# Kernel tuning notes

Hardware: AMD Instinct MI355X
Metric: run time of the kernel (lower is better)

The kernel has to match this reference:

```python
import jax, jax.numpy as jnp
import numpy as np

B, S, H, P = 8, 2048, 512, 16
K = H // 2

def setup_inputs() -> dict:
    key = jax.random.key(0)
    ks = jax.random.split(key, 6)
    sc_h = 1.0 / np.sqrt(H)
    sc_k = 1.0 / np.sqrt(K)
    return {
        "hidden_state": jax.random.normal(ks[0], (B, S, H), dtype=jnp.float32),
        "head_w": jax.random.normal(ks[1], (P, H), dtype=jnp.float32) * sc_h,
        "head_b": jnp.zeros((P,), dtype=jnp.float32),
        "embeds": jax.random.normal(ks[2], (P, H), dtype=jnp.float32),
        "w1": jax.random.normal(ks[3], (P, H, K), dtype=jnp.float32) * sc_h,
        "b1": jnp.zeros((P, K), dtype=jnp.float32),
        "w2": jax.random.normal(ks[4], (P, K, H), dtype=jnp.float32) * sc_k,
        "b2": jnp.zeros((P, H), dtype=jnp.float32),
    }

def reference(hidden_state, head_w, head_b, embeds, w1, b1, w2, b2):
    # Routing: pool over seq, linear head, softmax over programs -> (B, P)
    pooled = hidden_state.mean(axis=1)                      # (B, H)
    logits = jnp.einsum("bh,ph->bp", pooled, head_w) + head_b
    probs = jax.nn.softmax(logits, axis=-1)                  # (B, P)

    # Add program embedding per expert: (P, B, S, H)
    x = hidden_state[None, :, :, :] + embeds[:, None, None, :]
    # Expert MLP: Linear(H->K), exact GELU, Linear(K->H)
    mid = jax.nn.gelu(
        jnp.einsum("pbsh,phk->pbsk", x, w1) + b1[:, None, None, :],
        approximate=False,
    )
    adapted = jnp.einsum("pbsk,pkh->pbsh", mid, w2) + b2[:, None, None, :]
    # Weighted sum over programs with per-batch probs
    out = jnp.einsum("pbsh,bp->bsh", adapted, probs)         # (B, S, H)
    return out
```

## Files before the change

### kernel.cpp

```cpp
#include <hip/hip_runtime.h>
#include <hip/hip_bf16.h>
#include <stdint.h>

#define B_ 8
#define S_ 2048
#define H_ 512
#define P_ 16
#define K_ 256
#define M_TOT (B_*S_)
#define KCAT (P_*K_)

typedef short bf8v __attribute__((ext_vector_type(8)));
typedef float f4v  __attribute__((ext_vector_type(4)));

__device__ __align__(16) unsigned short g_hidden[M_TOT*H_];
__device__ __align__(16) unsigned short g_w1t[P_*K_*H_];
__device__ __align__(16) unsigned short g_w2cat[H_*KCAT];
__device__ __align__(16) unsigned short g_mid[(size_t)M_TOT*KCAT];
__device__ float g_bias1[P_*K_];
__device__ float g_probs[B_*P_];
__device__ float g_bias2w[B_*H_];

__device__ __forceinline__ unsigned short f2bf(float x){
  unsigned int u = __builtin_bit_cast(unsigned int, x);
  u += 0x7fffu + ((u >> 16) & 1u);
  return (unsigned short)(u >> 16);
}

__device__ __forceinline__ float gelu_prob(float x, float prob){
  float x2 = x*x;
  float t1 = 0.044715f*x;
  float u2 = fmaf(t1, x2, x);
  float e  = __expf(1.5957691216f*u2);
  float r  = __builtin_amdgcn_rcpf(e + 1.0f);
  float px = prob*x;
  return fmaf(-px, r, px);
}

__device__ __forceinline__ void gll16(const unsigned short* src, unsigned short* lds){
  __builtin_amdgcn_global_load_lds(
      (const __attribute__((address_space(1))) unsigned int*)src,
      (__attribute__((address_space(3))) unsigned int*)lds,
      16, 0, 0);
}

__global__ void cvt_pool(const float* __restrict__ hs, float* __restrict__ pooled){
  const int row0 = blockIdx.x * 64;
  const int b = row0 >> 11;
  const int tx = threadIdx.x & 127, ty = threadIdx.x >> 7;
  const float4* src = (const float4*)(hs + (size_t)row0*H_) + tx;
  ushort4* dst = (ushort4*)g_hidden + (size_t)row0*(H_/4) + tx;
  float4 s = {0.f,0.f,0.f,0.f};
  for (int r = ty; r < 64; r += 2){
    float4 v = src[(size_t)r*128];
    s.x += v.x; s.y += v.y; s.z += v.z; s.w += v.w;
    ushort4 o = {f2bf(v.x), f2bf(v.y), f2bf(v.z), f2bf(v.w)};
    dst[(size_t)r*128] = o;
  }
  __shared__ float4 red[256];
  red[threadIdx.x] = s;
  __syncthreads();
  if (ty == 0){
    float4 a = red[threadIdx.x], c = red[threadIdx.x + 128];
    atomicAdd(&pooled[b*H_ + tx*4 + 0], a.x + c.x);
    atomicAdd(&pooled[b*H_ + tx*4 + 1], a.y + c.y);
    atomicAdd(&pooled[b*H_ + tx*4 + 2], a.z + c.z);
    atomicAdd(&pooled[b*H_ + tx*4 + 3], a.w + c.w);
  }
}

__global__ void routing_kernel(const float* __restrict__ pooled,
                               const float* __restrict__ head_w,
                               const float* __restrict__ head_b,
                               const float* __restrict__ b2,
                               const float* __restrict__ b1){
  __shared__ float logits[B_][P_];
  __shared__ float sprob[B_][P_];
  int w = threadIdx.x >> 6, lane = threadIdx.x & 63;
  for (int idx = threadIdx.x; idx < P_*K_; idx += blockDim.x)
    g_bias1[idx] = b1[idx];
  for (int i = 0; i < 16; ++i){
    int pair = w*16 + i; int b = pair >> 4; int p = pair & 15;
    float acc = 0.0f;
    for (int h = lane; h < H_; h += 64) acc += pooled[b*H_+h]*head_w[p*H_+h];
    for (int off=32; off; off>>=1) acc += __shfl_down(acc, off);
    if (lane==0) logits[b][p] = acc * (1.0f/S_) + head_b[p];
  }
  __syncthreads();
  if (threadIdx.x < B_){
    int b = threadIdx.x;
    float mx = -1e30f;
    #pragma unroll
    for (int p=0;p<P_;++p) mx = fmaxf(mx, logits[b][p]);
    float e[P_]; float s = 0.0f;
    #pragma unroll
    for (int p=0;p<P_;++p){ e[p] = __expf(logits[b][p]-mx); s += e[p]; }
    float inv = 1.0f/s;
    #pragma unroll
    for (int p=0;p<P_;++p){ float pr = e[p]*inv; g_probs[b*P_+p] = pr; sprob[b][p] = pr; }
  }
  __syncthreads();
  for (int idx = threadIdx.x; idx < B_*H_; idx += blockDim.x){
    int b = idx >> 9, h = idx & (H_-1);
    float a = 0.0f;
    #pragma unroll
    for (int p=0;p<P_;++p) a += sprob[b][p]*b2[p*H_+h];
    g_bias2w[idx] = a;
  }
}

__global__ void transpose_cvt(const float* __restrict__ in, int R, int C, int which,
                              const float* __restrict__ embeds){
  int nrt = R >> 5, nct = C >> 5;
  int p   = blockIdx.x / (nrt*nct);
  int rem = blockIdx.x % (nrt*nct);
  int rt = rem / nct, ct = rem % nct;
  int tx = threadIdx.x & 31, ty = threadIdx.x >> 5;
  __shared__ float t[32][33];
  const float* ip = in + (size_t)p*R*C + (size_t)(rt*32 + ty)*C + ct*32 + tx;
  #pragma unroll
  for (int k=0;k<4;++k) t[ty + 8*k][tx] = ip[(size_t)8*k*C];
  __syncthreads();
  if (which == 0){
    unsigned short* op = g_w1t + (size_t)p*R*C + (size_t)(ct*32 + ty)*R + rt*32 + tx;
    #pragma unroll
    for (int k=0;k<4;++k) op[(size_t)8*k*R] = f2bf(t[tx][ty + 8*k]);
    if (ty == 0){
      float s = 0.0f;
      const float* ep = embeds + p*H_ + rt*32;
      #pragma unroll 8
      for (int hh=0; hh<32; ++hh) s = fmaf(ep[hh], t[hh][tx], s);
      atomicAdd(&g_bias1[p*K_ + ct*32 + tx], s);
    }
  } else {
    unsigned short* op = g_w2cat + (size_t)(ct*32 + ty)*KCAT + p*K_ + rt*32 + tx;
    #pragma unroll
    for (int k=0;k<4;++k) op[(size_t)8*k*KCAT] = f2bf(t[tx][ty + 8*k]);
  }
}


__device__ __forceinline__ void stage128(unsigned short* dst, const unsigned short* gsrc,
                                         int strideShorts, int koff, int tid){
  #pragma unroll
  for (int s = 0; s < 4; ++s){
    const int o   = (s*256 + tid)*8;
    const int row = o >> 6;
    const int ku  = (o & 63) >> 3;
    const int sku = ku ^ (row & 7);
    gll16(gsrc + (size_t)row*strideShorts + koff + sku*8, dst + o);
  }
}

__device__ __forceinline__ void kcompute(const unsigned short* Ab, const unsigned short* Bb,
    int rowA0, int rowB0, int l15, int lhi, f4v acc[4][4]){
  #pragma unroll
  for (int ksub=0; ksub<2; ++ksub){
    const int kb = ksub*64 + lhi*16;
    bf8v aF[4], bF[4];
    #pragma unroll
    for (int t=0; t<4; ++t){
      const int ra = rowA0 + t*16 + l15;
      aF[t] = *(const bf8v*)((const char*)Ab + ra*128 + (kb ^ ((ra&7)<<4)));
      const int rb = rowB0 + t*16 + l15;
      bF[t] = *(const bf8v*)((const char*)Bb + rb*128 + (kb ^ ((rb&7)<<4)));
    }
    __builtin_amdgcn_s_setprio(1);
    #pragma unroll
    for (int mt=0; mt<4; ++mt)
      #pragma unroll
      for (int nt=0; nt<4; ++nt)
        acc[mt][nt] = __builtin_amdgcn_mfma_f32_16x16x32_bf16(aF[mt], bF[nt], acc[mt][nt], 0,0,0);
    __builtin_amdgcn_s_setprio(0);
  }
}

__global__ __launch_bounds__(256, 2) void l1_kernel(){
  __shared__ __align__(16) unsigned short lds[4*128*64];
  const int bid = blockIdx.x;
  const int xcd = bid & 7, i = bid >> 3;
  const int n0 = (xcd*4 + (i&3)) * 128;
  const int m0 = (i >> 2) * 128;
  const int p = n0 >> 8;
  const int b = m0 >> 11;
  const int tid = threadIdx.x, w = tid >> 6, lane = tid & 63;
  const int wm = w >> 1, wn = w & 1, l15 = lane & 15, lhi = lane >> 4;
  const unsigned short* gA = g_hidden + (size_t)m0 * H_;
  const unsigned short* gB = g_w1t + (size_t)n0 * H_;

  f4v acc[4][4];
  #pragma unroll
  for (int a=0;a<4;++a)
    #pragma unroll
    for (int c=0;c<4;++c) acc[a][c] = {0.f,0.f,0.f,0.f};

  stage128(lds, gA, H_, 0, tid);
  stage128(lds + 16384, gB, H_, 0, tid);
  __syncthreads();
  for (int kt = 0; kt < 8; ++kt){
    const int cur = kt & 1;
    unsigned short* An = lds + (cur ? 0 : 8192);
    unsigned short* Bn = lds + 16384 + (cur ? 0 : 8192);
    const unsigned short* Ac = lds + (cur ? 8192 : 0);
    const unsigned short* Bc = lds + 16384 + (cur ? 8192 : 0);
    if (kt < 7){
      stage128(An, gA, H_, (kt+1)*64, tid);
      stage128(Bn, gB, H_, (kt+1)*64, tid);
    }
    kcompute(Ac, Bc, wm*64, wn*64, l15, lhi, acc);
    __syncthreads();
  }

  const float prob = g_probs[b*P_ + p];
  #pragma unroll
  for (int nt=0; nt<4; ++nt){
    const int col = wn*64 + nt*16 + l15;
    const float bias = g_bias1[n0 + col];
    #pragma unroll
    for (int mt=0; mt<4; ++mt){
      #pragma unroll
      for (int j=0;j<4;++j){
        const int row = wm*64 + mt*16 + lhi*4 + j;
        float v = acc[mt][nt][j] + bias;
        lds[row*136 + col] = f2bf(gelu_prob(v, prob));
      }
    }
  }
  __syncthreads();
  const int cc = tid & 15, rr = tid >> 4;
  #pragma unroll
  for (int pass=0; pass<8; ++pass){
    const int row = pass*16 + rr;
    bf8v vv = *(const bf8v*)&lds[row*136 + cc*8];
    *(bf8v*)&g_mid[(size_t)(m0+row)*KCAT + n0 + cc*8] = vv;
  }
}

__global__ __launch_bounds__(256, 2) void l2_kernel(float* __restrict__ out){
  __shared__ __align__(16) unsigned short lds[4*128*64];
  const int bid = blockIdx.x;
  const int xcd = bid & 7, i = bid >> 3;
  const int n0 = (i & 3) * 128;
  const int m0 = (xcd*16 + (i >> 2)) * 128;
  const int b = m0 >> 11;
  const int tid = threadIdx.x, w = tid >> 6, lane = tid & 63;
  const int wm = w >> 1, wn = w & 1, l15 = lane & 15, lhi = lane >> 4;
  const unsigned short* gA = g_mid + (size_t)m0 * KCAT;
  const unsigned short* gB = g_w2cat + (size_t)n0 * KCAT;

  f4v acc[4][4];
  #pragma unroll
  for (int a=0;a<4;++a)
    #pragma unroll
    for (int c=0;c<4;++c) acc[a][c] = {0.f,0.f,0.f,0.f};

  stage128(lds, gA, KCAT, 0, tid);
  stage128(lds + 16384, gB, KCAT, 0, tid);
  __syncthreads();
  for (int kt = 0; kt < 64; ++kt){
    const int cur = kt & 1;
    unsigned short* An = lds + (cur ? 0 : 8192);
    unsigned short* Bn = lds + 16384 + (cur ? 0 : 8192);
    const unsigned short* Ac = lds + (cur ? 8192 : 0);
    const unsigned short* Bc = lds + 16384 + (cur ? 8192 : 0);
    if (kt < 63){
      stage128(An, gA, KCAT, (kt+1)*64, tid);
      stage128(Bn, gB, KCAT, (kt+1)*64, tid);
    }
    kcompute(Ac, Bc, wm*64, wn*64, l15, lhi, acc);
    __syncthreads();
  }

  #pragma unroll
  for (int nt=0; nt<4; ++nt){
    const int col = n0 + wn*64 + nt*16 + l15;
    const float extra = g_bias2w[b*H_ + col];
    #pragma unroll
    for (int mt=0; mt<4; ++mt){
      #pragma unroll
      for (int j=0;j<4;++j){
        const int row = m0 + wm*64 + mt*16 + lhi*4 + j;
        out[(size_t)row*H_ + col] = acc[mt][nt][j] + extra;
      }
    }
  }
}

extern "C" void kernel_launch(void* const* d_in, const int* in_sizes, int n_in,
                              void* d_out, int out_size, void* d_ws, size_t ws_size,
                              hipStream_t stream){
  const float* hidden = (const float*)d_in[0];
  const float* head_w = (const float*)d_in[1];
  const float* head_b = (const float*)d_in[2];
  const float* embeds = (const float*)d_in[3];
  const float* w1     = (const float*)d_in[4];
  const float* b1     = (const float*)d_in[5];
  const float* w2     = (const float*)d_in[6];
  const float* b2     = (const float*)d_in[7];
  float* out = (float*)d_out;
  float* pooled = (float*)d_ws;
  (void)in_sizes; (void)n_in; (void)out_size; (void)ws_size;

  (void)hipMemsetAsync(pooled, 0, B_*H_*sizeof(float), stream);
  cvt_pool      <<<M_TOT/64, 256, 0, stream>>>(hidden, pooled);
  routing_kernel<<<1, 512, 0, stream>>>(pooled, head_w, head_b, b2, b1);
  transpose_cvt <<<P_*(H_/32)*(K_/32), 256, 0, stream>>>(w1, H_, K_, 0, embeds);
  transpose_cvt <<<P_*(K_/32)*(H_/32), 256, 0, stream>>>(w2, K_, H_, 1, embeds);
  l1_kernel     <<<4096, 256, 0, stream>>>();
  l2_kernel     <<<512, 256, 0, stream>>>(out);
}
```

Baseline: 255.0 us.

## Single-buffer l1 for higher occupancy, fine-grained waitcnt in l2, fold bias2 into l2

```diff
diff --git a/kernel.cpp b/kernel.cpp
--- a/kernel.cpp
+++ b/kernel.cpp
@@ -19,7 +19,6 @@
 __device__ __align__(16) unsigned short g_mid[(size_t)M_TOT*KCAT];
 __device__ float g_bias1[P_*K_];
 __device__ float g_probs[B_*P_];
-__device__ float g_bias2w[B_*H_];
 
 __device__ __forceinline__ unsigned short f2bf(float x){
   unsigned int u = __builtin_bit_cast(unsigned int, x);
@@ -72,10 +71,8 @@
 __global__ void routing_kernel(const float* __restrict__ pooled,
                                const float* __restrict__ head_w,
                                const float* __restrict__ head_b,
-                               const float* __restrict__ b2,
                                const float* __restrict__ b1){
   __shared__ float logits[B_][P_];
-  __shared__ float sprob[B_][P_];
   int w = threadIdx.x >> 6, lane = threadIdx.x & 63;
   for (int idx = threadIdx.x; idx < P_*K_; idx += blockDim.x)
     g_bias1[idx] = b1[idx];
@@ -97,15 +94,7 @@
     for (int p=0;p<P_;++p){ e[p] = __expf(logits[b][p]-mx); s += e[p]; }
     float inv = 1.0f/s;
     #pragma unroll
-    for (int p=0;p<P_;++p){ float pr = e[p]*inv; g_probs[b*P_+p] = pr; sprob[b][p] = pr; }
-  }
-  __syncthreads();
-  for (int idx = threadIdx.x; idx < B_*H_; idx += blockDim.x){
-    int b = idx >> 9, h = idx & (H_-1);
-    float a = 0.0f;
-    #pragma unroll
-    for (int p=0;p<P_;++p) a += sprob[b][p]*b2[p*H_+h];
-    g_bias2w[idx] = a;
+    for (int p=0;p<P_;++p) g_probs[b*P_+p] = e[p]*inv;
   }
 }
 
@@ -175,8 +164,8 @@
   }
 }
 
-__global__ __launch_bounds__(256, 2) void l1_kernel(){
-  __shared__ __align__(16) unsigned short lds[4*128*64];
+__global__ __launch_bounds__(256, 4) void l1_kernel(){
+  __shared__ __align__(16) unsigned short lds[128*136];
   const int bid = blockIdx.x;
   const int xcd = bid & 7, i = bid >> 3;
   const int n0 = (xcd*4 + (i&3)) * 128;
@@ -194,20 +183,11 @@
     #pragma unroll
     for (int c=0;c<4;++c) acc[a][c] = {0.f,0.f,0.f,0.f};
 
-  stage128(lds, gA, H_, 0, tid);
-  stage128(lds + 16384, gB, H_, 0, tid);
-  __syncthreads();
   for (int kt = 0; kt < 8; ++kt){
-    const int cur = kt & 1;
-    unsigned short* An = lds + (cur ? 0 : 8192);
-    unsigned short* Bn = lds + 16384 + (cur ? 0 : 8192);
-    const unsigned short* Ac = lds + (cur ? 8192 : 0);
-    const unsigned short* Bc = lds + 16384 + (cur ? 8192 : 0);
-    if (kt < 7){
-      stage128(An, gA, H_, (kt+1)*64, tid);
-      stage128(Bn, gB, H_, (kt+1)*64, tid);
-    }
-    kcompute(Ac, Bc, wm*64, wn*64, l15, lhi, acc);
+    stage128(lds,        gA, H_, kt*64, tid);
+    stage128(lds + 8192, gB, H_, kt*64, tid);
+    __syncthreads();
+    kcompute(lds, lds + 8192, wm*64, wn*64, l15, lhi, acc);
     __syncthreads();
   }
 
@@ -236,7 +216,8 @@
   }
 }
 
-__global__ __launch_bounds__(256, 2) void l2_kernel(float* __restrict__ out){
+__global__ __launch_bounds__(256, 2) void l2_kernel(float* __restrict__ out,
+                                                   const float* __restrict__ b2){
   __shared__ __align__(16) unsigned short lds[4*128*64];
   const int bid = blockIdx.x;
   const int xcd = bid & 7, i = bid >> 3;
@@ -254,27 +235,32 @@
     #pragma unroll
     for (int c=0;c<4;++c) acc[a][c] = {0.f,0.f,0.f,0.f};
 
-  stage128(lds, gA, KCAT, 0, tid);
+  stage128(lds + 0,     gA, KCAT, 0, tid);
   stage128(lds + 16384, gB, KCAT, 0, tid);
-  __syncthreads();
   for (int kt = 0; kt < 64; ++kt){
     const int cur = kt & 1;
-    unsigned short* An = lds + (cur ? 0 : 8192);
-    unsigned short* Bn = lds + 16384 + (cur ? 0 : 8192);
-    const unsigned short* Ac = lds + (cur ? 8192 : 0);
-    const unsigned short* Bc = lds + 16384 + (cur ? 8192 : 0);
     if (kt < 63){
-      stage128(An, gA, KCAT, (kt+1)*64, tid);
-      stage128(Bn, gB, KCAT, (kt+1)*64, tid);
-    }
-    kcompute(Ac, Bc, wm*64, wn*64, l15, lhi, acc);
-    __syncthreads();
-  }
-
+      stage128(lds + (cur ? 0 : 8192),         gA, KCAT, (kt+1)*64, tid);
+      stage128(lds + 16384 + (cur ? 0 : 8192), gB, KCAT, (kt+1)*64, tid);
+      asm volatile("s_waitcnt vmcnt(8)" ::: "memory");
+    } else {
+      asm volatile("s_waitcnt vmcnt(0)" ::: "memory");
+    }
+    __builtin_amdgcn_s_barrier();
+    kcompute(lds + (cur ? 8192 : 0), lds + 16384 + (cur ? 8192 : 0),
+             wm*64, wn*64, l15, lhi, acc);
+    __builtin_amdgcn_s_barrier();
+  }
+
+  float pr[P_];
+  #pragma unroll
+  for (int pp=0; pp<P_; ++pp) pr[pp] = g_probs[b*P_ + pp];
   #pragma unroll
   for (int nt=0; nt<4; ++nt){
     const int col = n0 + wn*64 + nt*16 + l15;
-    const float extra = g_bias2w[b*H_ + col];
+    float extra = 0.0f;
+    #pragma unroll
+    for (int pp=0; pp<P_; ++pp) extra = fmaf(pr[pp], b2[pp*H_ + col], extra);
     #pragma unroll
     for (int mt=0; mt<4; ++mt){
       #pragma unroll
@@ -303,9 +289,9 @@
 
   (void)hipMemsetAsync(pooled, 0, B_*H_*sizeof(float), stream);
   cvt_pool      <<<M_TOT/64, 256, 0, stream>>>(hidden, pooled);
-  routing_kernel<<<1, 512, 0, stream>>>(pooled, head_w, head_b, b2, b1);
+  routing_kernel<<<1, 512, 0, stream>>>(pooled, head_w, head_b, b1);
   transpose_cvt <<<P_*(H_/32)*(K_/32), 256, 0, stream>>>(w1, H_, K_, 0, embeds);
   transpose_cvt <<<P_*(K_/32)*(H_/32), 256, 0, stream>>>(w2, K_, H_, 1, embeds);
   l1_kernel     <<<4096, 256, 0, stream>>>();
-  l2_kernel     <<<512, 256, 0, stream>>>(out);
-}
+  l2_kernel     <<<512, 256, 0, stream>>>(out, b2);
+}
```

Measured after the change: 250.4 us. Within noise of the previous version (-1.8%).
